# Kernel tuning notes

Hardware: AMD Instinct MI355X
Metric: run time of the kernel (lower is better)

The kernel has to match this reference:

```python
import jax, jax.numpy as jnp
import numpy as np

N_EMBD = 2048
NUM_GROUPS = 8
EXPERTS_PER_GROUP = 8
ROUTER_TEMPERATURE = 1.0
N_TOKENS = 16384


def setup_inputs() -> dict:
    key = jax.random.key(0)
    kx, kg, ke = jax.random.split(key, 3)
    x = jax.random.normal(kx, (N_TOKENS, N_EMBD), dtype=jnp.float32)
    # nn.Linear(in, out, bias=False) stores weight as [out, in]; kaiming-uniform-ish scale
    bound = 1.0 / np.sqrt(N_EMBD)
    group_gate_w = jax.random.uniform(kg, (NUM_GROUPS, N_EMBD), dtype=jnp.float32,
                                      minval=-bound, maxval=bound)
    expert_gate_w = jax.random.uniform(ke, (NUM_GROUPS * EXPERTS_PER_GROUP, N_EMBD),
                                       dtype=jnp.float32, minval=-bound, maxval=bound)
    return {"x": x, "group_gate_w": group_gate_w, "expert_gate_w": expert_gate_w}


def reference(x, group_gate_w, expert_gate_w):
    N = x.shape[0]
    G = NUM_GROUPS
    E_g = EXPERTS_PER_GROUP
    inv_temp = 1.0 / ROUTER_TEMPERATURE

    # Level 1: group routing
    group_logits = jnp.einsum('nd,gd->ng', x, group_gate_w)            # [N, G]
    group_probs = jax.nn.softmax(group_logits * inv_temp, axis=-1)     # [N, G]
    group_mask = group_probs >= (1.0 / G)                              # [N, G]

    # Level 2: expert routing within each group
    expert_logits = jnp.einsum('nd,ed->ne', x, expert_gate_w)          # [N, G*E_g]
    expert_logits = expert_logits.reshape(N, G, E_g)
    expert_probs = jax.nn.softmax(expert_logits * inv_temp, axis=-1)   # [N, G, E_g]
    expert_mask = expert_probs >= (1.0 / E_g)                          # [N, G, E_g]

    valid_mask_3d = group_mask[:, :, None] & expert_mask               # [N, G, E_g]
    selected_weights_3d = (group_probs[:, :, None] * expert_probs) * valid_mask_3d.astype(x.dtype)

    valid_mask = valid_mask_3d.reshape(N, G * E_g)
    selected_weights = selected_weights_3d.reshape(N, G * E_g)
    weight_sum = jnp.clip(jnp.sum(selected_weights, axis=-1, keepdims=True), 1e-9, None)
    normalized_weights = selected_weights / weight_sum
    return (valid_mask, normalized_weights)
```

## Files before the change

### kernel.cpp

```cpp
#include <hip/hip_runtime.h>
#include <hip/hip_bf16.h>


#define NT 16384
#define NE 2048
#define KC 128
#define NCHUNK 16

#define QS    272
#define PL    1088
#define FP    2208
#define XB    44160
#define BUFSZ 79488
#define LDS_BYTES 158976

typedef _Float16 v8h __attribute__((ext_vector_type(8)));
typedef float    v4f __attribute__((ext_vector_type(4)));

__global__ __launch_bounds__(512, 2)
void router(const float* __restrict__ x, const float* __restrict__ gw,
            const float* __restrict__ ew, float* __restrict__ out)
{
    __shared__ __align__(16) char sm[LDS_BYTES];
    const int tid  = threadIdx.x;
    const int lane = tid & 63;
    const int w    = tid >> 6;
    const int t0   = blockIdx.x * 64;

    const float* wsrc[3]; int who[3]; int wmode[3];
    #pragma unroll
    for (int i = 0; i < 3; ++i) {
        int s = tid + i * 512;
        if (s >= 1280) { wmode[i] = 0; wsrc[i] = ew; who[i] = 0; continue; }
        int gate = s >> 4, kslot = s & 15;
        int ks = kslot >> 2, q = kslot & 3;
        who[i] = ((gate >> 4) * 4 + ks) * FP + q * QS + (gate & 15) * 16;
        if (gate < 64)      { wmode[i] = 2; wsrc[i] = ew + (size_t)gate * NE + kslot * 8; }
        else if (gate < 72) { wmode[i] = 2; wsrc[i] = gw + (size_t)(gate - 64) * NE + kslot * 8; }
        else                { wmode[i] = 1; wsrc[i] = ew; }
    }
    const float* xsrc[2]; int xho[2];
    #pragma unroll
    for (int i = 0; i < 2; ++i) {
        int s = tid + i * 512;
        int token = s >> 4, kslot = s & 15;
        int ks = kslot >> 2, q = kslot & 3;
        xho[i] = XB + ((token >> 4) * 4 + ks) * FP + q * QS + (token & 15) * 16;
        xsrc[i] = x + (size_t)(t0 + token) * NE + kslot * 8;
    }

    float4 wr[3][2], xr[2][2];

    auto stage_load = [&](int c) {
        const int kc = c * KC;
        #pragma unroll
        for (int i = 0; i < 3; ++i) {
            if (wmode[i] == 2) {
                wr[i][0] = *(const float4*)(wsrc[i] + kc);
                wr[i][1] = *(const float4*)(wsrc[i] + kc + 4);
            } else {
                wr[i][0] = make_float4(0.f, 0.f, 0.f, 0.f);
                wr[i][1] = make_float4(0.f, 0.f, 0.f, 0.f);
            }
        }
        #pragma unroll
        for (int i = 0; i < 2; ++i) {
            xr[i][0] = *(const float4*)(xsrc[i] + kc);
            xr[i][1] = *(const float4*)(xsrc[i] + kc + 4);
        }
    };

    auto split8 = [](const float4& a, const float4& b, v8h& h, v8h& l) {
        float v[8] = {a.x, a.y, a.z, a.w, b.x, b.y, b.z, b.w};
        #pragma unroll
        for (int j = 0; j < 8; ++j) {
            _Float16 hh = (_Float16)v[j];
            h[j] = hh;
            l[j] = (_Float16)((v[j] - (float)hh) * 2048.0f);
        }
    };

    auto stage_commit = [&](int buf) {
        const int bb = buf * BUFSZ;
        #pragma unroll
        for (int i = 0; i < 3; ++i) {
            if (wmode[i] == 0) continue;
            v8h h, l;
            split8(wr[i][0], wr[i][1], h, l);
            *(v8h*)(sm + bb + who[i])      = h;
            *(v8h*)(sm + bb + who[i] + PL) = l;
        }
        #pragma unroll
        for (int i = 0; i < 2; ++i) {
            v8h h, l;
            split8(xr[i][0], xr[i][1], h, l);
            *(v8h*)(sm + bb + xho[i])      = h;
            *(v8h*)(sm + bb + xho[i] + PL) = l;
        }
    };

    const int tt = w & 3, s2 = w >> 2;
    v4f accHH[5], accC[5];
    #pragma unroll
    for (int g = 0; g < 5; ++g) { accHH[g] = (v4f)(0.f); accC[g] = (v4f)(0.f); }
    const int rdo = (lane >> 4) * QS + (lane & 15) * 16;

    stage_load(0);
    stage_commit(0);
    for (int c = 0; c < NCHUNK; ++c) {
        if (c + 1 < NCHUNK) stage_load(c + 1);
        __syncthreads();
        {
            const int bb = (c & 1) * BUFSZ;
            #pragma unroll
            for (int ksl = 0; ksl < 2; ++ksl) {
                const int ks = s2 * 2 + ksl;
                const char* xb = sm + bb + XB + (tt * 4 + ks) * FP + rdo;
                v8h Bh = *(const v8h*)xb;
                v8h Bl = *(const v8h*)(xb + PL);
                #pragma unroll
                for (int g = 0; g < 5; ++g) {
                    const char* wb = sm + bb + (g * 4 + ks) * FP + rdo;
                    v8h Ah = *(const v8h*)wb;
                    v8h Al = *(const v8h*)(wb + PL);
                    accHH[g] = __builtin_amdgcn_mfma_f32_16x16x32_f16(Ah, Bh, accHH[g], 0, 0, 0);
                    accC[g]  = __builtin_amdgcn_mfma_f32_16x16x32_f16(Ah, Bl, accC[g], 0, 0, 0);
                    accC[g]  = __builtin_amdgcn_mfma_f32_16x16x32_f16(Al, Bh, accC[g], 0, 0, 0);
                }
            }
        }
        if (c + 1 < NCHUNK) stage_commit((c + 1) & 1);
    }
    __syncthreads();

    float part[5][4];
    #pragma unroll
    for (int g = 0; g < 5; ++g)
        #pragma unroll
        for (int r = 0; r < 4; ++r)
            part[g][r] = accHH[g][r] + accC[g][r] * (1.0f / 2048.0f);

    float* red = (float*)sm;
    if (w >= 4) {
        #pragma unroll
        for (int g = 0; g < 5; ++g)
            #pragma unroll
            for (int r = 0; r < 4; ++r)
                red[((tt * 5 + g) * 4 + r) * 64 + lane] = part[g][r];
    }
    __syncthreads();
    float* la = (float*)(sm + 24576);
    if (w < 4) {
        #pragma unroll
        for (int g = 0; g < 5; ++g)
            #pragma unroll
            for (int r = 0; r < 4; ++r) {
                float v = part[g][r] + red[((tt * 5 + g) * 4 + r) * 64 + lane];
                int gate  = g * 16 + (lane >> 4) * 4 + r;
                int token = tt * 16 + (lane & 15);
                la[token * 80 + gate] = v;
            }
    }
    __syncthreads();

    if (tid < 64) {
        const float* lg = la + tid * 80;
        float* M = (float*)(sm + 45056) + tid * 64;
        float* W = (float*)(sm + 61440) + tid * 64;

        float gpb[8];
        float gmax = lg[64];
        #pragma unroll
        for (int g = 1; g < 8; ++g) gmax = fmaxf(gmax, lg[64 + g]);
        float gsum = 0.f;
        #pragma unroll
        for (int g = 0; g < 8; ++g) { gpb[g] = __expf(lg[64 + g] - gmax); gsum += gpb[g]; }
        const float ginv = 1.f / gsum;

        float sel[64];
        float wsum = 0.f;
        #pragma unroll
        for (int g = 0; g < 8; ++g) {
            const float gp_ = gpb[g] * ginv;
            float emax = lg[g * 8];
            #pragma unroll
            for (int j = 1; j < 8; ++j) emax = fmaxf(emax, lg[g * 8 + j]);
            float ep[8]; float esum = 0.f;
            #pragma unroll
            for (int j = 0; j < 8; ++j) { ep[j] = __expf(lg[g * 8 + j] - emax); esum += ep[j]; }
            const float einv = 1.f / esum;
            const bool gm = gp_ >= 0.125f;
            #pragma unroll
            for (int j = 0; j < 8; ++j) {
                const float pe = ep[j] * einv;
                const bool v = gm && (pe >= 0.125f);
                const float ww = v ? gp_ * pe : 0.f;
                M[g * 8 + j] = v ? 1.f : 0.f;
                sel[g * 8 + j] = ww;
                wsum += ww;
            }
        }
        const float inv = 1.f / fmaxf(wsum, 1e-9f);
        #pragma unroll
        for (int e = 0; e < 64; ++e) W[e] = sel[e] * inv;
    }
    __syncthreads();

    const float4* M4 = (const float4*)(sm + 45056);
    const float4* W4 = (const float4*)(sm + 61440);
    float4* o0 = (float4*)(out + (size_t)t0 * 64);
    float4* o1 = (float4*)(out + (size_t)NT * 64 + (size_t)t0 * 64);
    o0[tid]       = M4[tid];
    o0[tid + 512] = M4[tid + 512];
    o1[tid]       = W4[tid];
    o1[tid + 512] = W4[tid + 512];
}

extern "C" void kernel_launch(void* const* d_in, const int* in_sizes, int n_in,
                              void* d_out, int out_size, void* d_ws, size_t ws_size,
                              hipStream_t stream) {
    const float* x  = (const float*)d_in[0];
    const float* gw = (const float*)d_in[1];
    const float* ew = (const float*)d_in[2];
    float* out = (float*)d_out;
    (void)d_ws; (void)ws_size;

    router<<<dim3(NT / 64), dim3(512), 0, stream>>>(x, gw, ew, out);
}
```

Before: 201.8 us.

## Load x fragments directly into registers and shrink blocks to 32 tokens

Each block now handles 32 tokens with 256 threads. Activation fragments go straight from global memory into MFMA B-operand registers instead of through LDS, so only the gate weights are staged in LDS, using an XOR-swizzled layout in place of padding. This halves LDS use per block, so more blocks can be resident, and removes the x LDS round-trip. The cost is that the weight tile is now loaded and converted by twice as many blocks, which adds weight traffic and fp16 splitting work.

```diff
diff --git a/kernel.cpp b/kernel.cpp
--- a/kernel.cpp
+++ b/kernel.cpp
@@ -1,23 +1,19 @@
 #include <hip/hip_runtime.h>
-#include <hip/hip_bf16.h>
 
 
 #define NT 16384
 #define NE 2048
-#define KC 128
 #define NCHUNK 16
-
-#define QS    272
-#define PL    1088
-#define FP    2208
-#define XB    44160
-#define BUFSZ 79488
-#define LDS_BYTES 158976
+#define TOK 32
+#define NTH 256
+#define TILE 2048
+#define BUFSZ 40960
+#define LDS_BYTES 81920
 
 typedef _Float16 v8h __attribute__((ext_vector_type(8)));
 typedef float    v4f __attribute__((ext_vector_type(4)));
 
-__global__ __launch_bounds__(512, 2)
+__global__ __launch_bounds__(NTH, 2)
 void router(const float* __restrict__ x, const float* __restrict__ gw,
             const float* __restrict__ ew, float* __restrict__ out)
 {
@@ -25,37 +21,40 @@
     const int tid  = threadIdx.x;
     const int lane = tid & 63;
     const int w    = tid >> 6;
-    const int t0   = blockIdx.x * 64;
-
-    const float* wsrc[3]; int who[3]; int wmode[3];
-    #pragma unroll
-    for (int i = 0; i < 3; ++i) {
-        int s = tid + i * 512;
-        if (s >= 1280) { wmode[i] = 0; wsrc[i] = ew; who[i] = 0; continue; }
+    const int t0   = blockIdx.x * TOK;
+
+    const float* wsrc[5]; int who[5]; int wz[5];
+    #pragma unroll
+    for (int i = 0; i < 5; ++i) {
+        int s = tid + i * NTH;
         int gate = s >> 4, kslot = s & 15;
         int ks = kslot >> 2, q = kslot & 3;
-        who[i] = ((gate >> 4) * 4 + ks) * FP + q * QS + (gate & 15) * 16;
-        if (gate < 64)      { wmode[i] = 2; wsrc[i] = ew + (size_t)gate * NE + kslot * 8; }
-        else if (gate < 72) { wmode[i] = 2; wsrc[i] = gw + (size_t)(gate - 64) * NE + kslot * 8; }
-        else                { wmode[i] = 1; wsrc[i] = ew; }
-    }
-    const float* xsrc[2]; int xho[2];
-    #pragma unroll
-    for (int i = 0; i < 2; ++i) {
-        int s = tid + i * 512;
-        int token = s >> 4, kslot = s & 15;
-        int ks = kslot >> 2, q = kslot & 3;
-        xho[i] = XB + ((token >> 4) * 4 + ks) * FP + q * QS + (token & 15) * 16;
-        xsrc[i] = x + (size_t)(t0 + token) * NE + kslot * 8;
-    }
-
-    float4 wr[3][2], xr[2][2];
-
-    auto stage_load = [&](int c) {
-        const int kc = c * KC;
-        #pragma unroll
-        for (int i = 0; i < 3; ++i) {
-            if (wmode[i] == 2) {
+        int m = gate & 15, g = gate >> 4;
+        int swz = (q ^ (ks << 1)) & 7;
+        who[i] = (g * 4 + ks) * TILE + (((q * 16 + m) ^ swz) << 4);
+        if (gate < 64)      { wz[i] = 0; wsrc[i] = ew + (size_t)gate * NE + kslot * 8; }
+        else if (gate < 72) { wz[i] = 0; wsrc[i] = gw + (size_t)(gate - 64) * NE + kslot * 8; }
+        else                { wz[i] = 1; wsrc[i] = ew; }
+    }
+
+    const int tt = w >> 1, s2 = w & 1;
+    const float* xp = x + (size_t)(t0 + tt * 16 + (lane & 15)) * NE + (lane >> 4) * 8;
+
+    int rdk[2];
+    #pragma unroll
+    for (int ksl = 0; ksl < 2; ++ksl) {
+        int ks = s2 * 2 + ksl;
+        int swz = ((lane >> 4) ^ (ks << 1)) & 7;
+        rdk[ksl] = ks * TILE + ((lane ^ swz) << 4);
+    }
+
+    float4 wr[5][2], xr[2][2];
+
+    auto wload = [&](int c) {
+        const int kc = c * 128;
+        #pragma unroll
+        for (int i = 0; i < 5; ++i) {
+            if (!wz[i]) {
                 wr[i][0] = *(const float4*)(wsrc[i] + kc);
                 wr[i][1] = *(const float4*)(wsrc[i] + kc + 4);
             } else {
@@ -63,13 +62,15 @@
                 wr[i][1] = make_float4(0.f, 0.f, 0.f, 0.f);
             }
         }
-        #pragma unroll
-        for (int i = 0; i < 2; ++i) {
-            xr[i][0] = *(const float4*)(xsrc[i] + kc);
-            xr[i][1] = *(const float4*)(xsrc[i] + kc + 4);
-        }
-    };
-
+    };
+    auto xload = [&](int c) {
+        #pragma unroll
+        for (int ksl = 0; ksl < 2; ++ksl) {
+            const float* p = xp + c * 128 + (s2 * 2 + ksl) * 32;
+            xr[ksl][0] = *(const float4*)(p);
+            xr[ksl][1] = *(const float4*)(p + 4);
+        }
+    };
     auto split8 = [](const float4& a, const float4& b, v8h& h, v8h& l) {
         float v[8] = {a.x, a.y, a.z, a.w, b.x, b.y, b.z, b.w};
         #pragma unroll
@@ -79,57 +80,44 @@
             l[j] = (_Float16)((v[j] - (float)hh) * 2048.0f);
         }
     };
-
-    auto stage_commit = [&](int buf) {
+    auto wcommit = [&](int buf) {
         const int bb = buf * BUFSZ;
         #pragma unroll
-        for (int i = 0; i < 3; ++i) {
-            if (wmode[i] == 0) continue;
+        for (int i = 0; i < 5; ++i) {
             v8h h, l;
             split8(wr[i][0], wr[i][1], h, l);
-            *(v8h*)(sm + bb + who[i])      = h;
-            *(v8h*)(sm + bb + who[i] + PL) = l;
-        }
-        #pragma unroll
-        for (int i = 0; i < 2; ++i) {
-            v8h h, l;
-            split8(xr[i][0], xr[i][1], h, l);
-            *(v8h*)(sm + bb + xho[i])      = h;
-            *(v8h*)(sm + bb + xho[i] + PL) = l;
-        }
-    };
-
-    const int tt = w & 3, s2 = w >> 2;
+            *(v8h*)(sm + bb + who[i])        = h;
+            *(v8h*)(sm + bb + who[i] + 1024) = l;
+        }
+    };
+
     v4f accHH[5], accC[5];
     #pragma unroll
     for (int g = 0; g < 5; ++g) { accHH[g] = (v4f)(0.f); accC[g] = (v4f)(0.f); }
-    const int rdo = (lane >> 4) * QS + (lane & 15) * 16;
-
-    stage_load(0);
-    stage_commit(0);
+
+    wload(0); xload(0);
+    wcommit(0);
+    v8h Bh[2], Bl[2];
     for (int c = 0; c < NCHUNK; ++c) {
-        if (c + 1 < NCHUNK) stage_load(c + 1);
+        #pragma unroll
+        for (int ksl = 0; ksl < 2; ++ksl)
+            split8(xr[ksl][0], xr[ksl][1], Bh[ksl], Bl[ksl]);
+        if (c + 1 < NCHUNK) { xload(c + 1); wload(c + 1); }
         __syncthreads();
-        {
-            const int bb = (c & 1) * BUFSZ;
-            #pragma unroll
-            for (int ksl = 0; ksl < 2; ++ksl) {
-                const int ks = s2 * 2 + ksl;
-                const char* xb = sm + bb + XB + (tt * 4 + ks) * FP + rdo;
-                v8h Bh = *(const v8h*)xb;
-                v8h Bl = *(const v8h*)(xb + PL);
-                #pragma unroll
-                for (int g = 0; g < 5; ++g) {
-                    const char* wb = sm + bb + (g * 4 + ks) * FP + rdo;
-                    v8h Ah = *(const v8h*)wb;
-                    v8h Al = *(const v8h*)(wb + PL);
-                    accHH[g] = __builtin_amdgcn_mfma_f32_16x16x32_f16(Ah, Bh, accHH[g], 0, 0, 0);
-                    accC[g]  = __builtin_amdgcn_mfma_f32_16x16x32_f16(Ah, Bl, accC[g], 0, 0, 0);
-                    accC[g]  = __builtin_amdgcn_mfma_f32_16x16x32_f16(Al, Bh, accC[g], 0, 0, 0);
-                }
-            }
-        }
-        if (c + 1 < NCHUNK) stage_commit((c + 1) & 1);
+        const int bb = (c & 1) * BUFSZ;
+        #pragma unroll
+        for (int ksl = 0; ksl < 2; ++ksl) {
+            #pragma unroll
+            for (int g = 0; g < 5; ++g) {
+                const char* ab = sm + bb + g * (4 * TILE) + rdk[ksl];
+                v8h Ah = *(const v8h*)(ab);
+                v8h Al = *(const v8h*)(ab + 1024);
+                accHH[g] = __builtin_amdgcn_mfma_f32_16x16x32_f16(Ah, Bh[ksl], accHH[g], 0, 0, 0);
+                accC[g]  = __builtin_amdgcn_mfma_f32_16x16x32_f16(Ah, Bl[ksl], accC[g], 0, 0, 0);
+                accC[g]  = __builtin_amdgcn_mfma_f32_16x16x32_f16(Al, Bh[ksl], accC[g], 0, 0, 0);
+            }
+        }
+        if (c + 1 < NCHUNK) wcommit((c + 1) & 1);
     }
     __syncthreads();
 
@@ -141,7 +129,7 @@
             part[g][r] = accHH[g][r] + accC[g][r] * (1.0f / 2048.0f);
 
     float* red = (float*)sm;
-    if (w >= 4) {
+    if (s2 == 1) {
         #pragma unroll
         for (int g = 0; g < 5; ++g)
             #pragma unroll
@@ -149,8 +137,8 @@
                 red[((tt * 5 + g) * 4 + r) * 64 + lane] = part[g][r];
     }
     __syncthreads();
-    float* la = (float*)(sm + 24576);
-    if (w < 4) {
+    float* la = (float*)(sm + 10240);
+    if (s2 == 0) {
         #pragma unroll
         for (int g = 0; g < 5; ++g)
             #pragma unroll
@@ -158,15 +146,16 @@
                 float v = part[g][r] + red[((tt * 5 + g) * 4 + r) * 64 + lane];
                 int gate  = g * 16 + (lane >> 4) * 4 + r;
                 int token = tt * 16 + (lane & 15);
-                la[token * 80 + gate] = v;
-            }
-    }
-    __syncthreads();
-
-    if (tid < 64) {
-        const float* lg = la + tid * 80;
-        float* M = (float*)(sm + 45056) + tid * 64;
-        float* W = (float*)(sm + 61440) + tid * 64;
+                la[token * 84 + gate] = v;
+            }
+    }
+    __syncthreads();
+
+    if (lane < 8) {
+        const int token = w * 8 + lane;
+        const float* lg = la + token * 84;
+        float* M  = (float*)(sm + 20992) + token * 64;
+        float* Wn = (float*)(sm + 29184) + token * 64;
 
         float gpb[8];
         float gmax = lg[64];
@@ -202,18 +191,18 @@
         }
         const float inv = 1.f / fmaxf(wsum, 1e-9f);
         #pragma unroll
-        for (int e = 0; e < 64; ++e) W[e] = sel[e] * inv;
-    }
-    __syncthreads();
-
-    const float4* M4 = (const float4*)(sm + 45056);
-    const float4* W4 = (const float4*)(sm + 61440);
+        for (int e = 0; e < 64; ++e) Wn[e] = sel[e] * inv;
+    }
+    __syncthreads();
+
+    const float4* M4 = (const float4*)(sm + 20992);
+    const float4* W4 = (const float4*)(sm + 29184);
     float4* o0 = (float4*)(out + (size_t)t0 * 64);
     float4* o1 = (float4*)(out + (size_t)NT * 64 + (size_t)t0 * 64);
     o0[tid]       = M4[tid];
-    o0[tid + 512] = M4[tid + 512];
+    o0[tid + 256] = M4[tid + 256];
     o1[tid]       = W4[tid];
-    o1[tid + 512] = W4[tid + 512];
+    o1[tid + 256] = W4[tid + 256];
 }
 
 extern "C" void kernel_launch(void* const* d_in, const int* in_sizes, int n_in,
@@ -225,5 +214,5 @@
     float* out = (float*)d_out;
     (void)d_ws; (void)ws_size;
 
-    router<<<dim3(NT / 64), dim3(512), 0, stream>>>(x, gw, ew, out);
+    router<<<dim3(NT / TOK), dim3(NTH), 0, stream>>>(x, gw, ew, out);
 }
```

Result: slower. 209.8 us (+4.0%).
